# Kernel optimization log

Hardware: AMD Instinct MI355X
Metric: run time of the kernel (lower is better)

The kernel has to match this reference:

```python
import jax, jax.numpy as jnp
import numpy as np

TOTAL_NODES = 131072
IN_FEA = 512
RANK = 256
NUM_GRAPHS = 1024


def setup_inputs() -> dict:
    key = jax.random.key(0)
    kx, kw, kb, ks = jax.random.split(key, 4)
    x = jax.random.normal(kx, (TOTAL_NODES, IN_FEA), dtype=jnp.float32)
    W = jax.random.normal(kw, (RANK, IN_FEA), dtype=jnp.float32) * (1.0 / np.sqrt(IN_FEA))
    b = jax.random.normal(kb, (RANK,), dtype=jnp.float32)
    segment_ids = jnp.sort(jax.random.randint(ks, (TOTAL_NODES,), 0, NUM_GRAPHS, dtype=jnp.int32))
    return {"x": x, "W": W, "b": b, "segment_ids": segment_ids, "num_segments": NUM_GRAPHS}


def reference(x, W, b, segment_ids, num_segments):
    # per-node projection + tanh: [total_nodes, rank]
    t = jnp.tanh(x @ W.T + b)
    # multiplicative reduction over the nodes of each graph -> [num_graphs, rank]
    return jax.ops.segment_prod(t, segment_ids, num_segments=num_segments)
```

## Files before the change

kernel.cpp:

```cpp
#include <hip/hip_runtime.h>
#include <hip/hip_bf16.h>
#include <stdint.h>

#define M_TOTAL 131072
#define K_DIM   512
#define N_RANK  256
#define NSEG    1024
#define KC      64
#define NKC     (K_DIM / KC)
#define BM      128
#define NBLK    (M_TOTAL / BM)
#define NB64    (M_TOTAL / 64)

typedef __attribute__((ext_vector_type(8))) short bf16x8;
typedef __attribute__((ext_vector_type(4))) float f32x4;

#define BAR() do { \
    asm volatile("s_waitcnt lgkmcnt(0)" ::: "memory"); \
    __builtin_amdgcn_s_barrier(); \
} while (0)

__device__ inline short f2b(float f) {
    __hip_bfloat16 h = __float2bfloat16(f);
    return __builtin_bit_cast(short, h);
}

__device__ inline float fast_tanh(float z) {
    float e = __expf(2.0f * fabsf(z));
    return copysignf(1.0f - 2.0f / (e + 1.0f), z);
}

__global__ void prep_kernel(const float* __restrict__ W,
                            __hip_bfloat16* __restrict__ Wb,
                            float* __restrict__ out) {
    int i = blockIdx.x * 256 + threadIdx.x;
    out[i] = 1.0f;
    if (i < N_RANK * K_DIM) Wb[i] = __float2bfloat16(W[i]);
}

__launch_bounds__(512, 4)
__global__ void fused_kernel(const float* __restrict__ x,
                             const __hip_bfloat16* __restrict__ Wb,
                             const float* __restrict__ bias,
                             const int* __restrict__ seg,
                             float* __restrict__ out,
                             float* __restrict__ partial) {
    const int tid  = threadIdx.x;
    const int wave = tid >> 6;
    const int lane = tid & 63;
    const int l16  = lane & 15;
    const int g    = lane >> 4;
    const int bid  = blockIdx.x;
    const int m0   = bid * BM;
    const int n0   = wave * 32;

    __shared__ alignas(16) char smem[32768];

    const int srow = tid >> 4;
    const int sc16 = tid & 15;

    f32x4 acc[8][2] = {};
    f32x4 sg[4];

    #define STAGE_LOAD(kc_)                                                   \
        do {                                                                  \
            _Pragma("unroll")                                                 \
            for (int it = 0; it < 4; ++it)                                    \
                sg[it] = *reinterpret_cast<const f32x4*>(                     \
                    x + (size_t)(m0 + it * 32 + srow) * K_DIM + (kc_) * KC + sc16 * 4); \
        } while (0)

    #define STAGE_WRITE(buf_)                                                 \
        do {                                                                  \
            _Pragma("unroll")                                                 \
            for (int it = 0; it < 4; ++it) {                                  \
                const int row = it * 32 + srow;                               \
                short4 p;                                                     \
                p.x = f2b(sg[it][0]); p.y = f2b(sg[it][1]);                   \
                p.z = f2b(sg[it][2]); p.w = f2b(sg[it][3]);                   \
                *reinterpret_cast<short4*>(smem + (buf_) * 16384 + row * 128  \
                    + ((sc16 * 8) ^ ((row & 7) << 4))) = p;                   \
            }                                                                 \
        } while (0)

    #define COMPUTE_SLICE(s_)                                                 \
        do {                                                                  \
            _Pragma("unroll")                                                 \
            for (int i = 0; i < 8; ++i) {                                     \
                const int row = i * 16 + l16;                                 \
                bf16x8 av = *reinterpret_cast<const bf16x8*>(                 \
                    smem + bufb + row * 128 +                                 \
                    (((s_) * 64 + g * 16) ^ ((row & 7) << 4)));               \
                _Pragma("unroll")                                             \
                for (int j = 0; j < 2; ++j)                                   \
                    acc[i][j] = __builtin_amdgcn_mfma_f32_16x16x32_bf16(      \
                        av, bfr[(s_)][j], acc[i][j], 0, 0, 0);                \
            }                                                                 \
        } while (0)

    STAGE_LOAD(0);
    asm volatile("s_waitcnt vmcnt(0)" ::: "memory");
    STAGE_WRITE(0);

    #pragma unroll
    for (int kc = 0; kc < NKC; ++kc) {
        BAR();

        bf16x8 bfr[2][2];
        #pragma unroll
        for (int s = 0; s < 2; ++s)
            #pragma unroll
            for (int j = 0; j < 2; ++j)
                bfr[s][j] = *reinterpret_cast<const bf16x8*>(
                    Wb + (size_t)(n0 + j * 16 + l16) * K_DIM + kc * KC + s * 32 + g * 8);
        __builtin_amdgcn_sched_barrier(0);

        if (kc + 1 < NKC) STAGE_LOAD(kc + 1);
        __builtin_amdgcn_sched_barrier(0);

        const int bufb = (kc & 1) * 16384;

        COMPUTE_SLICE(0);

        if (kc + 1 < NKC) {
            asm volatile("s_waitcnt vmcnt(0)" ::: "memory");
            STAGE_WRITE((kc + 1) & 1);
        }

        COMPUTE_SLICE(1);
    }
    #undef STAGE_LOAD
    #undef STAGE_WRITE
    #undef COMPUTE_SLICE

    #pragma unroll
    for (int j = 0; j < 2; ++j) {
        const float bj = bias[n0 + j * 16 + l16];
        #pragma unroll
        for (int i = 0; i < 8; ++i)
            #pragma unroll
            for (int r = 0; r < 4; ++r)
                acc[i][j][r] = fast_tanh(acc[i][j][r] + bj);
    }

    #pragma unroll
    for (int h = 0; h < 2; ++h) {
        const int vb     = bid * 2 + h;
        const int myseg  = seg[m0 + h * 64 + lane];
        const int prevsg = (lane == 0) ? (myseg ^ 1) : seg[m0 + h * 64 + lane - 1];
        uint64_t m = __ballot(myseg != prevsg);

        while (m) {
            const int start = (int)__builtin_ctzll(m);
            m &= m - 1;
            const int end = m ? (int)__builtin_ctzll(m) : 64;
            const int s   = __shfl(myseg, start);

            float p[2] = {1.0f, 1.0f};
            #pragma unroll
            for (int i2 = 0; i2 < 4; ++i2)
                #pragma unroll
                for (int r = 0; r < 4; ++r) {
                    const int row = i2 * 16 + g * 4 + r;
                    const bool in = (row >= start) && (row < end);
                    #pragma unroll
                    for (int j = 0; j < 2; ++j)
                        p[j] *= in ? acc[h * 4 + i2][j][r] : 1.0f;
                }
            #pragma unroll
            for (int j = 0; j < 2; ++j) {
                p[j] *= __shfl_xor(p[j], 16);
                p[j] *= __shfl_xor(p[j], 32);
            }
            if (g == 0) {
                #pragma unroll
                for (int j = 0; j < 2; ++j) {
                    const int col = n0 + j * 16 + l16;
                    if (start == 0)
                        partial[(size_t)(vb * 2 + 0) * N_RANK + col] = p[j];
                    else if (end == 64)
                        partial[(size_t)(vb * 2 + 1) * N_RANK + col] = p[j];
                    else
                        out[(size_t)s * N_RANK + col] = p[j];
                }
            }
        }
    }
}

__global__ void pass2_kernel(const int* __restrict__ seg,
                             const float* __restrict__ partial,
                             float* __restrict__ out) {
    const int b   = blockIdx.x;
    const int col = threadIdx.x;
    const int sF    = seg[b * 64];
    const int sL    = seg[b * 64 + 63];
    const int prevL = (b == 0) ? -1 : seg[b * 64 - 1];

    if (prevL < sF) {
        float p = partial[(size_t)(b * 2 + 0) * N_RANK + col];
        for (int b2 = b + 1; b2 < NB64 && seg[b2 * 64] == sF; ++b2)
            p *= partial[(size_t)(b2 * 2 + 0) * N_RANK + col];
        out[(size_t)sF * N_RANK + col] = p;
    }
    if (sL != sF) {
        float p = partial[(size_t)(b * 2 + 1) * N_RANK + col];
        for (int b2 = b + 1; b2 < NB64 && seg[b2 * 64] == sL; ++b2)
            p *= partial[(size_t)(b2 * 2 + 0) * N_RANK + col];
        out[(size_t)sL * N_RANK + col] = p;
    }
}

extern "C" void kernel_launch(void* const* d_in, const int* in_sizes, int n_in,
                              void* d_out, int out_size, void* d_ws, size_t ws_size,
                              hipStream_t stream) {
    const float* x   = (const float*)d_in[0];
    const float* W   = (const float*)d_in[1];
    const float* b   = (const float*)d_in[2];
    const int*   seg = (const int*)d_in[3];
    float*       out = (float*)d_out;
    __hip_bfloat16* Wb = (__hip_bfloat16*)d_ws;
    float* partial = (float*)((char*)d_ws + (1 << 20));

    prep_kernel<<<(NSEG * N_RANK) / 256, 256, 0, stream>>>(W, Wb, out);
    fused_kernel<<<NBLK, 512, 0, stream>>>(x, Wb, b, seg, out, partial);
    pass2_kernel<<<NB64, 256, 0, stream>>>(seg, partial, out);
}
```

Before: 82.08 us.

## Double K-chunk to 128 and split staging into two half-chunk phases

Raises the K chunk from 64 to 128, doubling the LDS staging buffers to 64KB, so the main loop runs 4 iterations instead of 8 with half as many barriers. Each iteration is split into two halves: W fragments for the half are loaded, the next chunk's x half is prefetched, two MFMA slices run, then the prefetched half is converted and written to LDS. The cost is twice the LDS per block (64KB), which likely limits how many 512-thread blocks fit per CU compared with the launch bound of 4, reducing occupancy and latency hiding.

After: 97.64 us. +18.9%, slower.

```diff
diff --git a/kernel.cpp b/kernel.cpp
--- a/kernel.cpp
+++ b/kernel.cpp
@@ -6,7 +6,7 @@
 #define K_DIM   512
 #define N_RANK  256
 #define NSEG    1024
-#define KC      64
+#define KC      128
 #define NKC     (K_DIM / KC)
 #define BM      128
 #define NBLK    (M_TOTAL / BM)
@@ -54,23 +54,25 @@
     const int m0   = bid * BM;
     const int n0   = wave * 32;
 
-    __shared__ alignas(16) char smem[32768];
+    __shared__ alignas(16) char smem[65536];
 
     const int srow = tid >> 4;
     const int sc16 = tid & 15;
 
     f32x4 acc[8][2] = {};
     f32x4 sg[4];
-
-    #define STAGE_LOAD(kc_)                                                   \
+    bf16x8 bfr[2][2];
+
+    #define STAGE_LOAD(kc_, h_)                                               \
         do {                                                                  \
             _Pragma("unroll")                                                 \
             for (int it = 0; it < 4; ++it)                                    \
                 sg[it] = *reinterpret_cast<const f32x4*>(                     \
-                    x + (size_t)(m0 + it * 32 + srow) * K_DIM + (kc_) * KC + sc16 * 4); \
-        } while (0)
-
-    #define STAGE_WRITE(buf_)                                                 \
+                    x + (size_t)(m0 + it * 32 + srow) * K_DIM + (kc_) * KC    \
+                      + (h_) * 64 + sc16 * 4);                                \
+        } while (0)
+
+    #define STAGE_WRITE(buf_, h_)                                             \
         do {                                                                  \
             _Pragma("unroll")                                                 \
             for (int it = 0; it < 4; ++it) {                                  \
@@ -78,9 +80,20 @@
                 short4 p;                                                     \
                 p.x = f2b(sg[it][0]); p.y = f2b(sg[it][1]);                   \
                 p.z = f2b(sg[it][2]); p.w = f2b(sg[it][3]);                   \
-                *reinterpret_cast<short4*>(smem + (buf_) * 16384 + row * 128  \
-                    + ((sc16 * 8) ^ ((row & 7) << 4))) = p;                   \
+                *reinterpret_cast<short4*>(smem + (buf_) * 32768 + row * 256  \
+                    + (((h_) * 128 + sc16 * 8) ^ ((row & 7) << 4))) = p;      \
             }                                                                 \
+        } while (0)
+
+    #define B_LOAD(sp_)                                                       \
+        do {                                                                  \
+            _Pragma("unroll")                                                 \
+            for (int s2 = 0; s2 < 2; ++s2)                                    \
+                _Pragma("unroll")                                             \
+                for (int j = 0; j < 2; ++j)                                   \
+                    bfr[s2][j] = *reinterpret_cast<const bf16x8*>(            \
+                        Wb + (size_t)(n0 + j * 16 + l16) * K_DIM + kc * KC    \
+                           + ((sp_) * 2 + s2) * 32 + g * 8);                  \
         } while (0)
 
     #define COMPUTE_SLICE(s_)                                                 \
@@ -89,48 +102,52 @@
             for (int i = 0; i < 8; ++i) {                                     \
                 const int row = i * 16 + l16;                                 \
                 bf16x8 av = *reinterpret_cast<const bf16x8*>(                 \
-                    smem + bufb + row * 128 +                                 \
+                    smem + bufb + row * 256 +                                 \
                     (((s_) * 64 + g * 16) ^ ((row & 7) << 4)));               \
                 _Pragma("unroll")                                             \
                 for (int j = 0; j < 2; ++j)                                   \
                     acc[i][j] = __builtin_amdgcn_mfma_f32_16x16x32_bf16(      \
-                        av, bfr[(s_)][j], acc[i][j], 0, 0, 0);                \
+                        av, bfr[(s_) & 1][j], acc[i][j], 0, 0, 0);            \
             }                                                                 \
         } while (0)
 
-    STAGE_LOAD(0);
+    STAGE_LOAD(0, 0);
     asm volatile("s_waitcnt vmcnt(0)" ::: "memory");
-    STAGE_WRITE(0);
+    STAGE_WRITE(0, 0);
+    STAGE_LOAD(0, 1);
+    asm volatile("s_waitcnt vmcnt(0)" ::: "memory");
+    STAGE_WRITE(0, 1);
 
     #pragma unroll
     for (int kc = 0; kc < NKC; ++kc) {
         BAR();
-
-        bf16x8 bfr[2][2];
-        #pragma unroll
-        for (int s = 0; s < 2; ++s)
-            #pragma unroll
-            for (int j = 0; j < 2; ++j)
-                bfr[s][j] = *reinterpret_cast<const bf16x8*>(
-                    Wb + (size_t)(n0 + j * 16 + l16) * K_DIM + kc * KC + s * 32 + g * 8);
-        __builtin_amdgcn_sched_barrier(0);
-
-        if (kc + 1 < NKC) STAGE_LOAD(kc + 1);
-        __builtin_amdgcn_sched_barrier(0);
-
-        const int bufb = (kc & 1) * 16384;
-
+        const int bufb = (kc & 1) * 32768;
+
+        B_LOAD(0);
+        __builtin_amdgcn_sched_barrier(0);
+        if (kc + 1 < NKC) STAGE_LOAD(kc + 1, 0);
+        __builtin_amdgcn_sched_barrier(0);
         COMPUTE_SLICE(0);
-
+        COMPUTE_SLICE(1);
         if (kc + 1 < NKC) {
             asm volatile("s_waitcnt vmcnt(0)" ::: "memory");
-            STAGE_WRITE((kc + 1) & 1);
+            STAGE_WRITE((kc + 1) & 1, 0);
         }
 
-        COMPUTE_SLICE(1);
+        B_LOAD(1);
+        __builtin_amdgcn_sched_barrier(0);
+        if (kc + 1 < NKC) STAGE_LOAD(kc + 1, 1);
+        __builtin_amdgcn_sched_barrier(0);
+        COMPUTE_SLICE(2);
+        COMPUTE_SLICE(3);
+        if (kc + 1 < NKC) {
+            asm volatile("s_waitcnt vmcnt(0)" ::: "memory");
+            STAGE_WRITE((kc + 1) & 1, 1);
+        }
     }
     #undef STAGE_LOAD
     #undef STAGE_WRITE
+    #undef B_LOAD
     #undef COMPUTE_SLICE
 
     #pragma unroll
```

## Deepen LDS ring to four stages with one barrier per two k-chunks

Applied to the files above, without the earlier changes.

Grows the shared-memory staging from two to four 16KB buffers. The main loop now handles two K chunks per barrier, prefetching chunk k+2 while computing chunk k, so the number of workgroup barriers is halved. It also raises wave priority around the MFMA blocks with s_setprio. The cost is doubling LDS to 64KB per block, which may limit how many 512-thread blocks fit per CU below the launch-bounds target of 4. The write-after-read ordering across the four buffers relies on a single barrier per pair of chunks.

Result: faster. 78.18 us, median of 2 (-4.8%).

```diff
diff --git a/kernel.cpp b/kernel.cpp
--- a/kernel.cpp
+++ b/kernel.cpp
@@ -54,7 +54,7 @@
     const int m0   = bid * BM;
     const int n0   = wave * 32;
 
-    __shared__ alignas(16) char smem[32768];
+    __shared__ alignas(16) char smem[65536];
 
     const int srow = tid >> 4;
     const int sc16 = tid & 15;
@@ -83,55 +83,74 @@
             }                                                                 \
         } while (0)
 
-    #define COMPUTE_SLICE(s_)                                                 \
-        do {                                                                  \
-            _Pragma("unroll")                                                 \
-            for (int i = 0; i < 8; ++i) {                                     \
-                const int row = i * 16 + l16;                                 \
-                bf16x8 av = *reinterpret_cast<const bf16x8*>(                 \
-                    smem + bufb + row * 128 +                                 \
-                    (((s_) * 64 + g * 16) ^ ((row & 7) << 4)));               \
+    #define B_LOAD(c_)                                                        \
+        do {                                                                  \
+            _Pragma("unroll")                                                 \
+            for (int s = 0; s < 2; ++s)                                       \
                 _Pragma("unroll")                                             \
                 for (int j = 0; j < 2; ++j)                                   \
-                    acc[i][j] = __builtin_amdgcn_mfma_f32_16x16x32_bf16(      \
-                        av, bfr[(s_)][j], acc[i][j], 0, 0, 0);                \
+                    bfr[s][j] = *reinterpret_cast<const bf16x8*>(             \
+                        Wb + (size_t)(n0 + j * 16 + l16) * K_DIM + (c_) * KC  \
+                           + s * 32 + g * 8);                                 \
+        } while (0)
+
+    #define COMPUTE(c_)                                                       \
+        do {                                                                  \
+            const int bufb = ((c_) & 3) * 16384;                              \
+            __builtin_amdgcn_s_setprio(1);                                    \
+            _Pragma("unroll")                                                 \
+            for (int s = 0; s < 2; ++s) {                                     \
+                _Pragma("unroll")                                             \
+                for (int i = 0; i < 8; ++i) {                                 \
+                    const int row = i * 16 + l16;                             \
+                    bf16x8 av = *reinterpret_cast<const bf16x8*>(             \
+                        smem + bufb + row * 128 +                             \
+                        ((s * 64 + g * 16) ^ ((row & 7) << 4)));              \
+                    _Pragma("unroll")                                         \
+                    for (int j = 0; j < 2; ++j)                               \
+                        acc[i][j] = __builtin_amdgcn_mfma_f32_16x16x32_bf16(  \
+                            av, bfr[s][j], acc[i][j], 0, 0, 0);               \
+                }                                                             \
             }                                                                 \
+            __builtin_amdgcn_s_setprio(0);                                    \
         } while (0)
 
     STAGE_LOAD(0);
     asm volatile("s_waitcnt vmcnt(0)" ::: "memory");
     STAGE_WRITE(0);
+    STAGE_LOAD(1);
+    asm volatile("s_waitcnt vmcnt(0)" ::: "memory");
+    STAGE_WRITE(1);
 
     #pragma unroll
-    for (int kc = 0; kc < NKC; ++kc) {
+    for (int kk = 0; kk < NKC; kk += 2) {
+        bf16x8 bfr[2][2];
         BAR();
 
-        bf16x8 bfr[2][2];
-        #pragma unroll
-        for (int s = 0; s < 2; ++s)
-            #pragma unroll
-            for (int j = 0; j < 2; ++j)
-                bfr[s][j] = *reinterpret_cast<const bf16x8*>(
-                    Wb + (size_t)(n0 + j * 16 + l16) * K_DIM + kc * KC + s * 32 + g * 8);
-        __builtin_amdgcn_sched_barrier(0);
-
-        if (kc + 1 < NKC) STAGE_LOAD(kc + 1);
-        __builtin_amdgcn_sched_barrier(0);
-
-        const int bufb = (kc & 1) * 16384;
-
-        COMPUTE_SLICE(0);
-
-        if (kc + 1 < NKC) {
+        B_LOAD(kk);
+        __builtin_amdgcn_sched_barrier(0);
+        if (kk + 2 < NKC) STAGE_LOAD(kk + 2);
+        __builtin_amdgcn_sched_barrier(0);
+        COMPUTE(kk);
+        if (kk + 2 < NKC) {
             asm volatile("s_waitcnt vmcnt(0)" ::: "memory");
-            STAGE_WRITE((kc + 1) & 1);
+            STAGE_WRITE((kk + 2) & 3);
         }
 
-        COMPUTE_SLICE(1);
+        B_LOAD(kk + 1);
+        __builtin_amdgcn_sched_barrier(0);
+        if (kk + 3 < NKC) STAGE_LOAD(kk + 3);
+        __builtin_amdgcn_sched_barrier(0);
+        COMPUTE(kk + 1);
+        if (kk + 3 < NKC) {
+            asm volatile("s_waitcnt vmcnt(0)" ::: "memory");
+            STAGE_WRITE((kk + 3) & 3);
+        }
     }
     #undef STAGE_LOAD
     #undef STAGE_WRITE
-    #undef COMPUTE_SLICE
+    #undef B_LOAD
+    #undef COMPUTE
 
     #pragma unroll
     for (int j = 0; j < 2; ++j) {
```
